# Kernel tuning notes

Measured on AMD Instinct MI355X. Metric: run time of the kernel, lower is better.

The kernel has to match this reference:

```python
import jax, jax.numpy as jnp
import numpy as np

D_MODEL = 512
STATE = 128
HALF = STATE // 2
SEQ = 4096
BATCH = 8


def setup_inputs() -> dict:
    key = jax.random.key(0)
    ks = jax.random.split(key, 4)
    u = jax.random.normal(ks[0], (BATCH, SEQ, D_MODEL), dtype=jnp.float32)
    # HiPPO init: Lambda = -0.5 + i*pi*n, n=1..HALF
    n = jnp.arange(1, HALF + 1, dtype=jnp.float32)
    log_Lambda_real = jnp.log(jnp.full((HALF,), 0.5, dtype=jnp.float32))  # log(-real) with real=-0.5
    Lambda_imag = jnp.pi * n
    B_real = jnp.ones((HALF, D_MODEL), dtype=jnp.float32)
    B_imag = jnp.zeros((HALF, D_MODEL), dtype=jnp.float32)
    C_real = jax.random.normal(ks[1], (D_MODEL, HALF), dtype=jnp.float32) / np.sqrt(STATE)
    C_imag = jax.random.normal(ks[2], (D_MODEL, HALF), dtype=jnp.float32) / np.sqrt(STATE)
    D = jax.random.normal(ks[3], (D_MODEL, D_MODEL), dtype=jnp.float32) / np.sqrt(D_MODEL)
    log_Delta = jnp.array([-3.0], dtype=jnp.float32)
    return {
        "u": u,
        "log_Lambda_real": log_Lambda_real,
        "Lambda_imag": Lambda_imag,
        "B_real": B_real,
        "B_imag": B_imag,
        "C_real": C_real,
        "C_imag": C_imag,
        "D": D,
        "log_Delta": log_Delta,
    }


def reference(u, log_Lambda_real, Lambda_imag, B_real, B_imag, C_real, C_imag, D, log_Delta):
    T = u.shape[1]
    Bc = B_real + 1j * B_imag            # (N/2, P) complex
    Cc = C_real + 1j * C_imag            # (P, N/2) complex
    # --- bilinear (Tustin) discretization ---
    Delta = jnp.exp(log_Delta)           # (1,)
    Lambda = -jnp.exp(jnp.clip(log_Lambda_real, -10.0, 10.0)) + 1j * Lambda_imag  # (N/2,)
    denom = 1.0 - (Delta / 2.0) * Lambda
    A_bar = (1.0 + (Delta / 2.0) * Lambda) / denom          # (N/2,)
    B_bar = (Delta / denom)[:, None] * Bc                   # (N/2, P)
    # --- FFT convolution with the SSM kernel k[n,t] = A_bar[n]^t ---
    t_idx = jnp.arange(T)
    k = jnp.exp(jnp.log(A_bar)[:, None] * t_idx[None, :])   # (N/2, T)
    u_c = u.astype(jnp.complex64)
    v = jnp.einsum('np,btp->bnt', B_bar, u_c)               # (B, N/2, T)
    fft_size = 2 * T
    V_f = jnp.fft.fft(v, n=fft_size, axis=-1)
    K_f = jnp.fft.fft(k, n=fft_size, axis=-1)
    conv = jnp.fft.ifft(V_f * K_f[None, :, :], axis=-1)[..., :T]  # (B, N/2, T)
    y = 2.0 * jnp.einsum('pn,bnt->btp', Cc, conv).real      # (B, T, P)
    return y + u @ D.T
```

## Files before the change

### kernel.cpp

```cpp
#include <hip/hip_runtime.h>
#include <hip/hip_bf16.h>
#include <stdint.h>


#define BATCH 8
#define SEQ   4096
#define DMODEL 512
#define HALF  64
#define CHUNK 64
#define NCHUNK (SEQ / CHUNK)
#define NT    10

typedef __attribute__((ext_vector_type(8))) short short8;
typedef __attribute__((ext_vector_type(4))) float f32x4;

__device__ __forceinline__ unsigned short f2bf(float f) {
    unsigned int u = __float_as_uint(f);
    u += 0x7fffu + ((u >> 16) & 1u);
    return (unsigned short)(u >> 16);
}
__device__ __forceinline__ float bf2f(unsigned short s) {
    return __uint_as_float((unsigned)s << 16);
}

#define GLOAD_LDS16(g, l)                                                    \
    __builtin_amdgcn_global_load_lds(                                        \
        (const __attribute__((address_space(1))) unsigned int*)(g),          \
        (__attribute__((address_space(3))) unsigned int*)(l), 16, 0, 0)


__global__ void k_consts(const float* __restrict__ logLr,
                         const float* __restrict__ Li_in,
                         const float* __restrict__ logDelta,
                         float* __restrict__ sr, float* __restrict__ si,
                         float* __restrict__ ApR, float* __restrict__ ApI) {
    int n = threadIdx.x;
    float Delta = expf(logDelta[0]);
    float llr = fminf(fmaxf(logLr[n], -10.f), 10.f);
    float Lr = -expf(llr);
    float Li = Li_in[n];
    float dr = 1.f - 0.5f * Delta * Lr;
    float di = -0.5f * Delta * Li;
    float dn = dr * dr + di * di;
    float nr = 1.f + 0.5f * Delta * Lr;
    float ni = 0.5f * Delta * Li;
    float Ar = (nr * dr + ni * di) / dn;
    float Ai = (ni * dr - nr * di) / dn;
    sr[n] = Delta * dr / dn;
    si[n] = -Delta * di / dn;
    float pr = 1.f, pi = 0.f;
    for (int k = 0; k <= CHUNK; ++k) {
        ApR[k * HALF + n] = pr;
        ApI[k * HALF + n] = pi;
        float npr = pr * Ar - pi * Ai;
        float npi = pr * Ai + pi * Ar;
        pr = npr; pi = npi;
    }
}

__global__ void k_build_Mv(const float* __restrict__ Br, const float* __restrict__ Bi,
                           const float* __restrict__ sr, const float* __restrict__ si,
                           unsigned short* __restrict__ Mv) {
    int np = blockIdx.x, p = threadIdx.x;
    int n = np & 63;
    float br = Br[n * DMODEL + p], bi = Bi[n * DMODEL + p];
    float v = (np < HALF) ? (sr[n] * br - si[n] * bi)
                          : (si[n] * br + sr[n] * bi);
    Mv[np * DMODEL + p] = f2bf(v);
}

__global__ void k_build_W(const float* __restrict__ Cr, const float* __restrict__ Ci,
                          const float* __restrict__ D, unsigned short* __restrict__ W) {
    int p = blockIdx.x, j = threadIdx.x;
    float v;
    if (j < HALF) v = 2.f * Cr[p * HALF + j];
    else if (j < 2 * HALF) v = -2.f * Ci[p * HALF + (j - HALF)];
    else v = D[p * DMODEL + (j - 2 * HALF)];
    W[p * 640 + j] = f2bf(v);
}


__global__ void k_scanA(const unsigned short* __restrict__ Vb,
                        const float* __restrict__ ApR, const float* __restrict__ ApI,
                        float* __restrict__ E) {
    int tid = threadIdx.x;
    int n = tid & 63;
    int c = ((blockIdx.x & 31) << 1) + (tid >> 6);
    int b = blockIdx.x >> 5;
    float Ar = ApR[HALF + n], Ai = ApI[HALF + n];
    float xr = 0.f, xi = 0.f;
    size_t base = ((size_t)b * SEQ + (size_t)c * CHUNK) * 128 + n;
    for (int tl = 0; tl < CHUNK; ++tl) {
        float vr = bf2f(Vb[base]), vi = bf2f(Vb[base + 64]);
        float nxr = Ar * xr - Ai * xi + vr;
        float nxi = Ar * xi + Ai * xr + vi;
        xr = nxr; xi = nxi;
        base += 128;
    }
    int eidx = ((b * NCHUNK + c) * 2) * HALF + n;
    E[eidx] = xr; E[eidx + 64] = xi;
}

__global__ void k_scanB(const float* __restrict__ E, float* __restrict__ Carry,
                        const float* __restrict__ ApR, const float* __restrict__ ApI) {
    int lane = threadIdx.x & 63;
    int wv = threadIdx.x >> 6;
    int b = blockIdx.x;
    for (int n = wv; n < HALF; n += 8) {
        float wr = ApR[CHUNK * HALF + n], wi = ApI[CHUNK * HALF + n];
        int idx = ((b * NCHUNK + lane) * 2) * HALF + n;
        float sR = E[idx], sI = E[idx + 64];
#pragma unroll
        for (int s = 1; s < 64; s <<= 1) {
            float pR = __shfl_up(sR, s, 64);
            float pI = __shfl_up(sI, s, 64);
            if (lane >= s) {
                sR += wr * pR - wi * pI;
                sI += wr * pI + wi * pR;
            }
            float nwr = wr * wr - wi * wi;
            float nwi = 2.f * wr * wi;
            wr = nwr; wi = nwi;
        }
        float cR = __shfl_up(sR, 1, 64);
        float cI = __shfl_up(sI, 1, 64);
        if (lane == 0) { cR = 0.f; cI = 0.f; }
        Carry[idx] = cR; Carry[idx + 64] = cI;
    }
}

__global__ void k_scanC(const unsigned short* __restrict__ Vb,
                        const float* __restrict__ Carry,
                        const float* __restrict__ ApR, const float* __restrict__ ApI,
                        unsigned short* __restrict__ Xb) {
    int tid = threadIdx.x;
    int n = tid & 63;
    int c = ((blockIdx.x & 31) << 1) + (tid >> 6);
    int b = blockIdx.x >> 5;
    int cidx = ((b * NCHUNK + c) * 2) * HALF + n;
    float xr = Carry[cidx], xi = Carry[cidx + 64];
    float Ar = ApR[HALF + n], Ai = ApI[HALF + n];
    size_t base = ((size_t)b * SEQ + (size_t)c * CHUNK) * 128 + n;
    for (int tl = 0; tl < CHUNK; ++tl) {
        float vr = bf2f(Vb[base]), vi = bf2f(Vb[base + 64]);
        float nxr = Ar * xr - Ai * xi + vr;
        float nxi = Ar * xi + Ai * xr + vi;
        xr = nxr; xi = nxi;
        Xb[base] = f2bf(xr); Xb[base + 64] = f2bf(xi);
        base += 128;
    }
}

__global__ __launch_bounds__(512) void gemm1(const float* __restrict__ U,
                                             const unsigned short* __restrict__ Mv,
                                             unsigned short* __restrict__ Vb,
                                             unsigned short* __restrict__ Ub) {
    __shared__ __align__(16) unsigned short Bs[128 * 512];
    const int tid = threadIdx.x;
    const int lane = tid & 63;
    const int w = tid >> 6;
    const int wm = w >> 1, wn = w & 1;
    const int l15 = lane & 15, l4 = lane >> 4;
    const int row0 = blockIdx.x * 128;

#pragma unroll
    for (int i = 0; i < 16; ++i) {
        int c = i * 512 + tid;
        int n = c >> 6;
        int p = c & 63;
        int ko = p ^ (n & 7);
        GLOAD_LDS16(Mv + (size_t)n * DMODEL + ko * 8, &Bs[(i * 512 + w * 64) * 8]);
    }
    asm volatile("s_waitcnt vmcnt(0)" ::: "memory");
    __builtin_amdgcn_s_barrier();
    __builtin_amdgcn_sched_barrier(0);

    f32x4 acc[2][4];
#pragma unroll
    for (int i = 0; i < 2; ++i)
#pragma unroll
        for (int j = 0; j < 4; ++j) acc[i][j] = (f32x4)(0.f);

#pragma unroll 2
    for (int k0 = 0; k0 < DMODEL; k0 += 32) {
        short8 af[2];
#pragma unroll
        for (int i = 0; i < 2; ++i) {
            int r = row0 + wm * 32 + i * 16 + l15;
            const float* ag = U + (size_t)r * DMODEL + k0 + l4 * 8;
            float4 a0 = ((const float4*)ag)[0];
            float4 a1 = ((const float4*)ag)[1];
            union { short8 s; uint4 u; } pk;
            pk.u.x = (unsigned)f2bf(a0.x) | ((unsigned)f2bf(a0.y) << 16);
            pk.u.y = (unsigned)f2bf(a0.z) | ((unsigned)f2bf(a0.w) << 16);
            pk.u.z = (unsigned)f2bf(a1.x) | ((unsigned)f2bf(a1.y) << 16);
            pk.u.w = (unsigned)f2bf(a1.z) | ((unsigned)f2bf(a1.w) << 16);
            af[i] = pk.s;
            if (wn == 0)
                *(uint4*)&Ub[(size_t)r * DMODEL + k0 + l4 * 8] = pk.u;
        }
        short8 bf[4];
#pragma unroll
        for (int j = 0; j < 4; ++j) {
            int n = wn * 64 + j * 16 + l15;
            int q = ((k0 >> 3) + l4) ^ (n & 7);
            bf[j] = *(const short8*)&Bs[n * DMODEL + q * 8];
        }
#pragma unroll
        for (int i = 0; i < 2; ++i)
#pragma unroll
            for (int j = 0; j < 4; ++j)
                acc[i][j] = __builtin_amdgcn_mfma_f32_16x16x32_bf16(af[i], bf[j], acc[i][j], 0, 0, 0);
    }

#pragma unroll
    for (int i = 0; i < 2; ++i) {
        int rbase = row0 + wm * 32 + i * 16 + l4 * 4;
#pragma unroll
        for (int j = 0; j < 4; ++j) {
            int col = wn * 64 + j * 16 + l15;
#pragma unroll
            for (int r = 0; r < 4; ++r)
                Vb[(size_t)(rbase + r) * 128 + col] = f2bf(acc[i][j][r]);
        }
    }
}


#define STAGE_K(t, kh, j) do {                                                 \
    int c_ = (kh) * 1024 + (j) * 512 + tid;                                    \
    int ct_ = c_ ^ (((c_ >> 5) & 1) << 1);                                     \
    int r_ = (ct_ >> 2) & 255;                                                 \
    int kcol_ = (t) * 64 + (kh) * 32 + (ct_ & 3) * 8;                          \
    const unsigned short* asrc_ = (kcol_ < 128)                                \
        ? Xb + (size_t)(row0 + r_) * 128 + kcol_                               \
        : Ub + (size_t)(row0 + r_) * 512 + (kcol_ - 128);                      \
    GLOAD_LDS16(asrc_, &As[((t) & 1) * 16384 + ((kh) * 1024 + (j) * 512 + w * 64) * 8]); \
    GLOAD_LDS16(W + (size_t)(col0 + r_) * 640 + kcol_,                         \
                &Bs[((t) & 1) * 16384 + ((kh) * 1024 + (j) * 512 + w * 64) * 8]); \
} while (0)

#define LDAB(t, kh) do {                                                       \
    _Pragma("unroll") for (int i_ = 0; i_ < 8; ++i_) {                         \
        int r_ = wm * 128 + i_ * 16 + l15;                                     \
        int c_ = (l4 * 8) ^ (((r_ >> 3) & 1) << 4);                            \
        af[i_] = *(const short8*)&As[((t) & 1) * 16384 + (kh) * 8192 + r_ * 32 + c_]; \
    }                                                                          \
    _Pragma("unroll") for (int j_ = 0; j_ < 4; ++j_) {                         \
        int r_ = wn * 64 + j_ * 16 + l15;                                      \
        int c_ = (l4 * 8) ^ (((r_ >> 3) & 1) << 4);                            \
        bf[j_] = *(const short8*)&Bs[((t) & 1) * 16384 + (kh) * 8192 + r_ * 32 + c_]; \
    } } while (0)

#define MFMA32() do {                                                          \
    __builtin_amdgcn_s_setprio(1);                                             \
    _Pragma("unroll") for (int i_ = 0; i_ < 8; ++i_)                           \
    _Pragma("unroll") for (int j_ = 0; j_ < 4; ++j_)                           \
        acc[i_][j_] = __builtin_amdgcn_mfma_f32_16x16x32_bf16(                 \
            af[i_], bf[j_], acc[i_][j_], 0, 0, 0);                             \
    __builtin_amdgcn_s_setprio(0);                                             \
} while (0)

__global__ __launch_bounds__(512) void gemm23_8p(const unsigned short* __restrict__ Xb,
                                                 const unsigned short* __restrict__ Ub,
                                                 const unsigned short* __restrict__ W,
                                                 float* __restrict__ C) {
    __shared__ __align__(16) unsigned short As[2 * 16384];
    __shared__ __align__(16) unsigned short Bs[2 * 16384];
    const int tid = threadIdx.x;
    const int lane = tid & 63;
    const int w = tid >> 6;
    const int wm = w >> 2, wn = w & 3;
    const int l15 = lane & 15, l4 = lane >> 4;

    int lin = blockIdx.y * gridDim.x + blockIdx.x;
    int sw = (lin & 7) * 32 + (lin >> 3);
    const int row0 = (sw & 127) * 256;
    const int col0 = (sw >> 7) * 256;

    f32x4 acc[8][4];
#pragma unroll
    for (int m = 0; m < 8; ++m)
#pragma unroll
        for (int n = 0; n < 4; ++n) acc[m][n] = (f32x4)(0.f);

    STAGE_K(0, 0, 0); STAGE_K(0, 0, 1);
    STAGE_K(0, 1, 0); STAGE_K(0, 1, 1);
    asm volatile("s_waitcnt vmcnt(4)" ::: "memory");
    __builtin_amdgcn_s_barrier();
    __builtin_amdgcn_sched_barrier(0);

    short8 af[8], bf[4];
    for (int t = 0; t < NT; ++t) {
        const bool pf = (t < NT - 1);
        LDAB(t, 0);
        if (pf) { STAGE_K(t + 1, 0, 0); STAGE_K(t + 1, 0, 1); }
        __builtin_amdgcn_s_barrier();
        __builtin_amdgcn_sched_barrier(0);
        MFMA32();
        if (pf) asm volatile("s_waitcnt vmcnt(4)" ::: "memory");
        else    asm volatile("s_waitcnt vmcnt(0)" ::: "memory");
        __builtin_amdgcn_s_barrier();
        __builtin_amdgcn_sched_barrier(0);
        LDAB(t, 1);
        if (pf) { STAGE_K(t + 1, 1, 0); STAGE_K(t + 1, 1, 1); }
        __builtin_amdgcn_s_barrier();
        __builtin_amdgcn_sched_barrier(0);
        MFMA32();
        if (pf) asm volatile("s_waitcnt vmcnt(4)" ::: "memory");
        __builtin_amdgcn_s_barrier();
        __builtin_amdgcn_sched_barrier(0);
    }

#pragma unroll
    for (int m = 0; m < 8; ++m) {
        int rbase = row0 + wm * 128 + m * 16 + l4 * 4;
#pragma unroll
        for (int n = 0; n < 4; ++n) {
            int col = col0 + wn * 64 + n * 16 + l15;
#pragma unroll
            for (int r = 0; r < 4; ++r)
                C[(size_t)(rbase + r) * DMODEL + col] = acc[m][n][r];
        }
    }
}


extern "C" void kernel_launch(void* const* d_in, const int* in_sizes, int n_in,
                              void* d_out, int out_size, void* d_ws, size_t ws_size,
                              hipStream_t stream) {
    const float* u      = (const float*)d_in[0];
    const float* logLr  = (const float*)d_in[1];
    const float* Li     = (const float*)d_in[2];
    const float* Br     = (const float*)d_in[3];
    const float* Bi     = (const float*)d_in[4];
    const float* Cr     = (const float*)d_in[5];
    const float* Ci     = (const float*)d_in[6];
    const float* D      = (const float*)d_in[7];
    const float* logDel = (const float*)d_in[8];
    float* out = (float*)d_out;

    const size_t M = (size_t)BATCH * SEQ;
    unsigned short* Vb = (unsigned short*)d_ws;
    unsigned short* Ub = Vb + M * 128;
    unsigned short* Xb = Ub + M * 512;
    unsigned short* Mv = Xb + M * 128;
    unsigned short* W  = Mv + 128 * 512;
    float* fp    = (float*)(W + 512 * 640);
    float* E     = fp;
    float* Carry = E + 65536;
    float* ApR   = Carry + 65536;
    float* ApI   = ApR + 4160;
    float* sr    = ApI + 4160;
    float* si    = sr + 64;

    hipLaunchKernelGGL(k_consts, dim3(1), dim3(64), 0, stream,
                       logLr, Li, logDel, sr, si, ApR, ApI);
    hipLaunchKernelGGL(k_build_Mv, dim3(128), dim3(512), 0, stream, Br, Bi, sr, si, Mv);
    hipLaunchKernelGGL(k_build_W, dim3(512), dim3(640), 0, stream, Cr, Ci, D, W);

    hipLaunchKernelGGL(gemm1, dim3(M / 128), dim3(512), 0, stream, u, Mv, Vb, Ub);

    hipLaunchKernelGGL(k_scanA, dim3(256), dim3(128), 0, stream, Vb, ApR, ApI, E);
    hipLaunchKernelGGL(k_scanB, dim3(BATCH), dim3(512), 0, stream, E, Carry, ApR, ApI);
    hipLaunchKernelGGL(k_scanC, dim3(256), dim3(128), 0, stream, Vb, Carry, ApR, ApI, Xb);

    hipLaunchKernelGGL(gemm23_8p, dim3(M / 256, DMODEL / 256), dim3(512), 0, stream,
                       Xb, Ub, W, out);
}
```

Measured before the change: 92.52 us.

## Retile gemm1 with small per-step LDS staging and deepen gemm23 prefetch pipeline

```diff
diff --git a/kernel.cpp b/kernel.cpp
--- a/kernel.cpp
+++ b/kernel.cpp
@@ -155,73 +155,62 @@
                                              const unsigned short* __restrict__ Mv,
                                              unsigned short* __restrict__ Vb,
                                              unsigned short* __restrict__ Ub) {
-    __shared__ __align__(16) unsigned short Bs[128 * 512];
+    __shared__ __align__(16) unsigned short As[64 * 32];
+    __shared__ __align__(16) unsigned short Bs[128 * 32];
     const int tid = threadIdx.x;
     const int lane = tid & 63;
     const int w = tid >> 6;
-    const int wm = w >> 1, wn = w & 1;
+    const int wm = w >> 2, wn = w & 3;
     const int l15 = lane & 15, l4 = lane >> 4;
-    const int row0 = blockIdx.x * 128;
-
-#pragma unroll
-    for (int i = 0; i < 16; ++i) {
-        int c = i * 512 + tid;
-        int n = c >> 6;
-        int p = c & 63;
-        int ko = p ^ (n & 7);
-        GLOAD_LDS16(Mv + (size_t)n * DMODEL + ko * 8, &Bs[(i * 512 + w * 64) * 8]);
-    }
-    asm volatile("s_waitcnt vmcnt(0)" ::: "memory");
-    __builtin_amdgcn_s_barrier();
-    __builtin_amdgcn_sched_barrier(0);
-
-    f32x4 acc[2][4];
-#pragma unroll
-    for (int i = 0; i < 2; ++i)
-#pragma unroll
-        for (int j = 0; j < 4; ++j) acc[i][j] = (f32x4)(0.f);
-
-#pragma unroll 2
+    const int row0 = blockIdx.x * 64;
+    const int srow = tid >> 3;
+    const int sh = (tid & 7) * 4;
+
+    f32x4 acc[2][2];
+#pragma unroll
+    for (int m = 0; m < 2; ++m)
+#pragma unroll
+        for (int n = 0; n < 2; ++n) acc[m][n] = (f32x4)(0.f);
+
     for (int k0 = 0; k0 < DMODEL; k0 += 32) {
-        short8 af[2];
-#pragma unroll
-        for (int i = 0; i < 2; ++i) {
-            int r = row0 + wm * 32 + i * 16 + l15;
-            const float* ag = U + (size_t)r * DMODEL + k0 + l4 * 8;
-            float4 a0 = ((const float4*)ag)[0];
-            float4 a1 = ((const float4*)ag)[1];
-            union { short8 s; uint4 u; } pk;
-            pk.u.x = (unsigned)f2bf(a0.x) | ((unsigned)f2bf(a0.y) << 16);
-            pk.u.y = (unsigned)f2bf(a0.z) | ((unsigned)f2bf(a0.w) << 16);
-            pk.u.z = (unsigned)f2bf(a1.x) | ((unsigned)f2bf(a1.y) << 16);
-            pk.u.w = (unsigned)f2bf(a1.z) | ((unsigned)f2bf(a1.w) << 16);
-            af[i] = pk.s;
-            if (wn == 0)
-                *(uint4*)&Ub[(size_t)r * DMODEL + k0 + l4 * 8] = pk.u;
-        }
-        short8 bf[4];
-#pragma unroll
-        for (int j = 0; j < 4; ++j) {
-            int n = wn * 64 + j * 16 + l15;
-            int q = ((k0 >> 3) + l4) ^ (n & 7);
-            bf[j] = *(const short8*)&Bs[n * DMODEL + q * 8];
-        }
-#pragma unroll
-        for (int i = 0; i < 2; ++i)
-#pragma unroll
-            for (int j = 0; j < 4; ++j)
-                acc[i][j] = __builtin_amdgcn_mfma_f32_16x16x32_bf16(af[i], bf[j], acc[i][j], 0, 0, 0);
-    }
-
-#pragma unroll
-    for (int i = 0; i < 2; ++i) {
-        int rbase = row0 + wm * 32 + i * 16 + l4 * 4;
-#pragma unroll
-        for (int j = 0; j < 4; ++j) {
-            int col = wn * 64 + j * 16 + l15;
+        const float4 av = *(const float4*)(U + (size_t)(row0 + srow) * DMODEL + k0 + sh);
+
+        __syncthreads();
+
+        GLOAD_LDS16(Mv + (size_t)(tid >> 2) * DMODEL + k0 + (tid & 3) * 8,
+                    &Bs[(w * 64) * 8]);
+
+        uint2 wa;
+        wa.x = (unsigned)f2bf(av.x) | ((unsigned)f2bf(av.y) << 16);
+        wa.y = (unsigned)f2bf(av.z) | ((unsigned)f2bf(av.w) << 16);
+        *(uint2*)&As[srow * 32 + sh] = wa;
+        *(uint2*)&Ub[(size_t)(row0 + srow) * DMODEL + k0 + sh] = wa;
+
+        __syncthreads();
+
+        short8 af[2], bf[2];
+#pragma unroll
+        for (int m = 0; m < 2; ++m)
+            af[m] = *(const short8*)&As[(wm * 32 + m * 16 + l15) * 32 + l4 * 8];
+#pragma unroll
+        for (int n = 0; n < 2; ++n)
+            bf[n] = *(const short8*)&Bs[(wn * 32 + n * 16 + l15) * 32 + l4 * 8];
+#pragma unroll
+        for (int m = 0; m < 2; ++m)
+#pragma unroll
+            for (int n = 0; n < 2; ++n)
+                acc[m][n] = __builtin_amdgcn_mfma_f32_16x16x32_bf16(af[m], bf[n], acc[m][n], 0, 0, 0);
+    }
+
+#pragma unroll
+    for (int m = 0; m < 2; ++m) {
+        int rbase = row0 + wm * 32 + m * 16 + l4 * 4;
+#pragma unroll
+        for (int n = 0; n < 2; ++n) {
+            int col = wn * 32 + n * 16 + l15;
 #pragma unroll
             for (int r = 0; r < 4; ++r)
-                Vb[(size_t)(rbase + r) * 128 + col] = f2bf(acc[i][j][r]);
+                Vb[(size_t)(rbase + r) * 128 + col] = f2bf(acc[m][n][r]);
         }
     }
 }
@@ -261,6 +250,12 @@
     __builtin_amdgcn_s_setprio(0);                                             \
 } while (0)
 
+#define PHASE_SYNC(N) do {                                                     \
+    asm volatile("s_waitcnt vmcnt(" #N ")" ::: "memory");                      \
+    __builtin_amdgcn_s_barrier();                                              \
+    __builtin_amdgcn_sched_barrier(0);                                         \
+} while (0)
+
 __global__ __launch_bounds__(512) void gemm23_8p(const unsigned short* __restrict__ Xb,
                                                  const unsigned short* __restrict__ Ub,
                                                  const unsigned short* __restrict__ W,
@@ -286,31 +281,25 @@
 
     STAGE_K(0, 0, 0); STAGE_K(0, 0, 1);
     STAGE_K(0, 1, 0); STAGE_K(0, 1, 1);
-    asm volatile("s_waitcnt vmcnt(4)" ::: "memory");
-    __builtin_amdgcn_s_barrier();
-    __builtin_amdgcn_sched_barrier(0);
+    STAGE_K(1, 0, 0); STAGE_K(1, 0, 1);
 
     short8 af[8], bf[4];
-    for (int t = 0; t < NT; ++t) {
-        const bool pf = (t < NT - 1);
+    for (int t = 0; t < NT - 1; ++t) {
+        PHASE_SYNC(8);
         LDAB(t, 0);
-        if (pf) { STAGE_K(t + 1, 0, 0); STAGE_K(t + 1, 0, 1); }
-        __builtin_amdgcn_s_barrier();
-        __builtin_amdgcn_sched_barrier(0);
+        STAGE_K(t + 1, 1, 0); STAGE_K(t + 1, 1, 1);
         MFMA32();
-        if (pf) asm volatile("s_waitcnt vmcnt(4)" ::: "memory");
-        else    asm volatile("s_waitcnt vmcnt(0)" ::: "memory");
-        __builtin_amdgcn_s_barrier();
-        __builtin_amdgcn_sched_barrier(0);
+        PHASE_SYNC(8);
         LDAB(t, 1);
-        if (pf) { STAGE_K(t + 1, 1, 0); STAGE_K(t + 1, 1, 1); }
-        __builtin_amdgcn_s_barrier();
-        __builtin_amdgcn_sched_barrier(0);
+        if (t < NT - 2) { STAGE_K(t + 2, 0, 0); STAGE_K(t + 2, 0, 1); }
         MFMA32();
-        if (pf) asm volatile("s_waitcnt vmcnt(4)" ::: "memory");
-        __builtin_amdgcn_s_barrier();
-        __builtin_amdgcn_sched_barrier(0);
-    }
+    }
+    PHASE_SYNC(4);
+    LDAB(NT - 1, 0);
+    MFMA32();
+    PHASE_SYNC(0);
+    LDAB(NT - 1, 1);
+    MFMA32();
 
 #pragma unroll
     for (int m = 0; m < 8; ++m) {
@@ -359,7 +348,7 @@
     hipLaunchKernelGGL(k_build_Mv, dim3(128), dim3(512), 0, stream, Br, Bi, sr, si, Mv);
     hipLaunchKernelGGL(k_build_W, dim3(512), dim3(640), 0, stream, Cr, Ci, D, W);
 
-    hipLaunchKernelGGL(gemm1, dim3(M / 128), dim3(512), 0, stream, u, Mv, Vb, Ub);
+    hipLaunchKernelGGL(gemm1, dim3(M / 64), dim3(512), 0, stream, u, Mv, Vb, Ub);
 
     hipLaunchKernelGGL(k_scanA, dim3(256), dim3(128), 0, stream, Vb, ApR, ApI, E);
     hipLaunchKernelGGL(k_scanB, dim3(BATCH), dim3(512), 0, stream, E, Carry, ApR, ApI);
```

Result: faster. 85.56 us (-7.5%).
